# Kernel optimization log

Hardware: AMD Instinct MI355X
Metric: run time of the kernel (lower is better)

Reference implementation:

```python
import jax, jax.numpy as jnp
import numpy as np
import math

HEAD_SIZE = 128
N_EMBED = 2048
B, T = 4, 4096
TOP_K_RATIO = 0.1


def setup_inputs() -> dict:
    key = jax.random.key(0)
    k1, k2, k3, k4 = jax.random.split(key, 4)
    index = jax.random.normal(k1, (B, T, N_EMBED), dtype=jnp.float32)
    s = 1.0 / math.sqrt(N_EMBED)
    Wq = jax.random.normal(k2, (N_EMBED, HEAD_SIZE), dtype=jnp.float32) * s
    Wk = jax.random.normal(k3, (N_EMBED, HEAD_SIZE), dtype=jnp.float32) * s
    Wv = jax.random.normal(k4, (N_EMBED, HEAD_SIZE), dtype=jnp.float32) * s
    return {"index": index, "Wq": Wq, "Wk": Wk, "Wv": Wv}


def reference(index, Wq, Wk, Wv):
    # memory = index (self-attention case)
    Bv, Tv, _ = index.shape
    top_k = int(TOP_K_RATIO * Tv)  # 409

    q = index @ Wq  # [B, T, D]
    k = index @ Wk
    v = index @ Wv

    q_norms = jnp.linalg.norm(q, axis=-1)  # [B, T]
    _, top_idx = jax.lax.top_k(q_norms, top_k)  # [B, K]

    idx = top_idx[..., None]  # [B, K, 1]
    q_topk = jnp.take_along_axis(q, idx, axis=1)  # [B, K, D]
    k_topk = jnp.take_along_axis(k, idx, axis=1)
    v_topk = jnp.take_along_axis(v, idx, axis=1)

    w = jnp.einsum('bid,bjd->bij', q_topk, k_topk) / math.sqrt(HEAD_SIZE)
    # eval mode: no causal mask (only applied in training), dropout = identity
    w = jax.nn.softmax(w, axis=-1)  # stable softmax (internal max subtraction)
    out_topk = w @ v_topk  # [B, K, D]

    batch_idx = jnp.arange(Bv)[:, None]  # [B, 1]
    output = jnp.zeros((Bv, Tv, HEAD_SIZE), dtype=out_topk.dtype)
    output = output.at[batch_idx, top_idx].add(out_topk)  # scatter_add (indices unique)
    return output
```

## Files before the change

### kernel.cpp

```cpp
#include <hip/hip_runtime.h>
#include <hip/hip_bf16.h>

#define NB 4
#define NT 4096
#define NC 2048
#define ND 128
#define NK 409
#define KPAD 416

#define BM 32
#define BK 32
#define ASTR 40
#define BSTR 40

typedef __attribute__((ext_vector_type(8))) short short8;
typedef __attribute__((ext_vector_type(4))) float f32x4;

__device__ __forceinline__ void split2(float x, ushort& h, ushort& l) {
    union { float f; unsigned u; } a; a.f = x;
    unsigned r = a.u + 0x7FFFu + ((a.u >> 16) & 1u);
    h = (ushort)(r >> 16);
    union { unsigned u; float f; } hb; hb.u = ((unsigned)h) << 16;
    float res = x - hb.f;
    union { float f; unsigned u; } b; b.f = res;
    unsigned r2 = b.u + 0x7FFFu + ((b.u >> 16) & 1u);
    l = (ushort)(r2 >> 16);
}

__device__ __forceinline__ uint2 pack4(const ushort* s) {
    uint2 v;
    v.x = (unsigned)s[0] | ((unsigned)s[1] << 16);
    v.y = (unsigned)s[2] | ((unsigned)s[3] << 16);
    return v;
}

__device__ __forceinline__ uint4 pack8(const ushort* s) {
    uint4 v;
    v.x = (unsigned)s[0] | ((unsigned)s[1] << 16);
    v.y = (unsigned)s[2] | ((unsigned)s[3] << 16);
    v.z = (unsigned)s[4] | ((unsigned)s[5] << 16);
    v.w = (unsigned)s[6] | ((unsigned)s[7] << 16);
    return v;
}

__global__ __launch_bounds__(256) void bconv_kernel(
    const float* __restrict__ Wq, ushort* __restrict__ Bhi, ushort* __restrict__ Blo)
{
    const int t = threadIdx.x;
    const int n = t & 127;
    const int kk0 = blockIdx.x * 32 + (t >> 7) * 16;
    ushort hb[16], lb[16];
    #pragma unroll
    for (int j = 0; j < 16; ++j) {
        float x = Wq[(size_t)(kk0 + j) * ND + n];
        split2(x, hb[j], lb[j]);
    }
    *(uint4*)&Bhi[(size_t)n * NC + kk0 + 0] = pack8(hb);
    *(uint4*)&Bhi[(size_t)n * NC + kk0 + 8] = pack8(hb + 8);
    *(uint4*)&Blo[(size_t)n * NC + kk0 + 0] = pack8(lb);
    *(uint4*)&Blo[(size_t)n * NC + kk0 + 8] = pack8(lb + 8);
}

__global__ __launch_bounds__(256) void bconv_kv_kernel(
    const float* __restrict__ Wk, const float* __restrict__ Wv,
    ushort* __restrict__ Bhi, ushort* __restrict__ Blo)
{
    const float* __restrict__ W = blockIdx.y ? Wv : Wk;
    const int t = threadIdx.x;
    const int n = t & 127;
    const int nr = blockIdx.y * 128 + n;
    const int kk0 = blockIdx.x * 32 + (t >> 7) * 16;
    ushort hb[16], lb[16];
    #pragma unroll
    for (int j = 0; j < 16; ++j) {
        float x = W[(size_t)(kk0 + j) * ND + n];
        split2(x, hb[j], lb[j]);
    }
    *(uint4*)&Bhi[(size_t)nr * NC + kk0 + 0] = pack8(hb);
    *(uint4*)&Bhi[(size_t)nr * NC + kk0 + 8] = pack8(hb + 8);
    *(uint4*)&Blo[(size_t)nr * NC + kk0 + 0] = pack8(lb);
    *(uint4*)&Blo[(size_t)nr * NC + kk0 + 8] = pack8(lb + 8);
}

__global__ __launch_bounds__(256, 2) void qgemm_mfma(
    const float* __restrict__ A, const ushort* __restrict__ Bhi,
    const ushort* __restrict__ Blo, float* __restrict__ q)
{
    __shared__ ushort Ah[BM * ASTR];
    __shared__ ushort Al[BM * ASTR];
    __shared__ ushort Bh[128 * BSTR];
    __shared__ ushort Bl[128 * BSTR];

    const int tid  = threadIdx.x;
    const int m0   = blockIdx.x * BM;
    const int w    = tid >> 6;
    const int lane = tid & 63;
    const int wm   = w >> 1, wn = w & 1;
    const int lrow = lane & 15, lq = lane >> 4;

    const int ar = tid >> 3, ak = (tid & 7) * 4;
    const float* aptr = A + (size_t)(m0 + ar) * NC + ak;
    const int br = tid >> 1, bk = (tid & 1) * 16;
    const ushort* bhp = Bhi + (size_t)br * NC + bk;
    const ushort* blp = Blo + (size_t)br * NC + bk;

    f32x4 acc[4];
    #pragma unroll
    for (int j = 0; j < 4; ++j) acc[j] = (f32x4){0.f, 0.f, 0.f, 0.f};

    for (int k0 = 0; k0 < NC; k0 += BK) {
        float4 f0 = *(const float4*)(aptr + k0);
        uint4 bh0 = *(const uint4*)(bhp + k0);
        uint4 bh1 = *(const uint4*)(bhp + k0 + 8);
        uint4 bl0 = *(const uint4*)(blp + k0);
        uint4 bl1 = *(const uint4*)(blp + k0 + 8);
        ushort h[4], l[4];
        split2(f0.x, h[0], l[0]);
        split2(f0.y, h[1], l[1]);
        split2(f0.z, h[2], l[2]);
        split2(f0.w, h[3], l[3]);

        __syncthreads();
        *(uint2*)&Ah[ar * ASTR + ak] = pack4(h);
        *(uint2*)&Al[ar * ASTR + ak] = pack4(l);
        *(uint4*)&Bh[br * BSTR + bk + 0] = bh0;
        *(uint4*)&Bh[br * BSTR + bk + 8] = bh1;
        *(uint4*)&Bl[br * BSTR + bk + 0] = bl0;
        *(uint4*)&Bl[br * BSTR + bk + 8] = bl1;
        __syncthreads();

        const int row = wm * 16 + lrow;
        short8 ah = *(const short8*)&Ah[row * ASTR + lq * 8];
        short8 al = *(const short8*)&Al[row * ASTR + lq * 8];
        #pragma unroll
        for (int ni = 0; ni < 4; ++ni) {
            const int n = wn * 64 + ni * 16 + lrow;
            short8 bhf = *(const short8*)&Bh[n * BSTR + lq * 8];
            short8 blf = *(const short8*)&Bl[n * BSTR + lq * 8];
            acc[ni] = __builtin_amdgcn_mfma_f32_16x16x32_bf16(ah, bhf, acc[ni], 0, 0, 0);
            acc[ni] = __builtin_amdgcn_mfma_f32_16x16x32_bf16(ah, blf, acc[ni], 0, 0, 0);
            acc[ni] = __builtin_amdgcn_mfma_f32_16x16x32_bf16(al, bhf, acc[ni], 0, 0, 0);
        }
    }

    #pragma unroll
    for (int ni = 0; ni < 4; ++ni) {
        const int col = wn * 64 + ni * 16 + lrow;
        #pragma unroll
        for (int r = 0; r < 4; ++r) {
            const int grow = m0 + wm * 16 + lq * 4 + r;
            q[(size_t)grow * ND + col] = acc[ni][r];
        }
    }
}

__global__ __launch_bounds__(256, 2) void kvgemm_mfma(
    const float* __restrict__ X, const ushort* __restrict__ Bhi,
    const ushort* __restrict__ Blo, const int* __restrict__ topi,
    float* __restrict__ ktop, float* __restrict__ vtop)
{
    __shared__ ushort Ah[BM * ASTR];
    __shared__ ushort Al[BM * ASTR];
    __shared__ ushort Bh[128 * BSTR];
    __shared__ ushort Bl[128 * BSTR];

    const int tid  = threadIdx.x;
    const int m0   = blockIdx.x * BM;
    const int w    = tid >> 6;
    const int lane = tid & 63;
    const int wm   = w >> 1, wn = w & 1;
    const int lrow = lane & 15, lq = lane >> 4;

    const int ar = tid >> 3, ak = (tid & 7) * 4;
    int gi = m0 + ar;
    int giC = gi < NB * NK ? gi : NB * NK - 1;
    int b = giC / NK, ii = giC % NK;
    int srow = topi[b * KPAD + ii];
    const float* aptr = X + ((size_t)b * NT + srow) * NC + ak;

    const int br = tid >> 1, bk = (tid & 1) * 16;
    const ushort* bhp = Bhi + (size_t)(blockIdx.y * 128 + br) * NC + bk;
    const ushort* blp = Blo + (size_t)(blockIdx.y * 128 + br) * NC + bk;

    f32x4 acc[4];
    #pragma unroll
    for (int j = 0; j < 4; ++j) acc[j] = (f32x4){0.f, 0.f, 0.f, 0.f};

    for (int k0 = 0; k0 < NC; k0 += BK) {
        float4 f0 = *(const float4*)(aptr + k0);
        uint4 bh0 = *(const uint4*)(bhp + k0);
        uint4 bh1 = *(const uint4*)(bhp + k0 + 8);
        uint4 bl0 = *(const uint4*)(blp + k0);
        uint4 bl1 = *(const uint4*)(blp + k0 + 8);
        ushort h[4], l[4];
        split2(f0.x, h[0], l[0]);
        split2(f0.y, h[1], l[1]);
        split2(f0.z, h[2], l[2]);
        split2(f0.w, h[3], l[3]);

        __syncthreads();
        *(uint2*)&Ah[ar * ASTR + ak] = pack4(h);
        *(uint2*)&Al[ar * ASTR + ak] = pack4(l);
        *(uint4*)&Bh[br * BSTR + bk + 0] = bh0;
        *(uint4*)&Bh[br * BSTR + bk + 8] = bh1;
        *(uint4*)&Bl[br * BSTR + bk + 0] = bl0;
        *(uint4*)&Bl[br * BSTR + bk + 8] = bl1;
        __syncthreads();

        const int row = wm * 16 + lrow;
        short8 ah = *(const short8*)&Ah[row * ASTR + lq * 8];
        short8 al = *(const short8*)&Al[row * ASTR + lq * 8];
        #pragma unroll
        for (int ni = 0; ni < 4; ++ni) {
            const int n = wn * 64 + ni * 16 + lrow;
            short8 bhf = *(const short8*)&Bh[n * BSTR + lq * 8];
            short8 blf = *(const short8*)&Bl[n * BSTR + lq * 8];
            acc[ni] = __builtin_amdgcn_mfma_f32_16x16x32_bf16(ah, bhf, acc[ni], 0, 0, 0);
            acc[ni] = __builtin_amdgcn_mfma_f32_16x16x32_bf16(ah, blf, acc[ni], 0, 0, 0);
            acc[ni] = __builtin_amdgcn_mfma_f32_16x16x32_bf16(al, bhf, acc[ni], 0, 0, 0);
        }
    }

    float* __restrict__ dst = blockIdx.y ? vtop : ktop;
    #pragma unroll
    for (int ni = 0; ni < 4; ++ni) {
        const int col = wn * 64 + ni * 16 + lrow;
        #pragma unroll
        for (int r = 0; r < 4; ++r) {
            const int grow = m0 + wm * 16 + lq * 4 + r;
            if (grow < NB * NK)
                dst[(size_t)grow * ND + col] = acc[ni][r];
        }
    }
}

__global__ __launch_bounds__(256) void qnorm_kernel(
    const float* __restrict__ q, float* __restrict__ qn)
{
    const int wv = (blockIdx.x * 256 + threadIdx.x) >> 6;
    const int lane = threadIdx.x & 63;
    const float* r = q + (size_t)wv * ND;
    float a = r[lane], b = r[lane + 64];
    float s = a * a + b * b;
    #pragma unroll
    for (int off = 32; off > 0; off >>= 1) s += __shfl_xor(s, off);
    if (lane == 0) qn[wv] = sqrtf(s);
}

__global__ __launch_bounds__(256) void topk_kernel(
    const float* __restrict__ qn, int* __restrict__ topi, int* __restrict__ cnt)
{
    __shared__ int rs[4][64];
    const int b = blockIdx.y;
    const int is = threadIdx.x & 63;
    const int i = blockIdx.x * 64 + is;
    const int chunk = threadIdx.x >> 6;
    const float vi = qn[(size_t)b * NT + i];
    const float4* qv = (const float4*)(qn + (size_t)b * NT + chunk * 1024);
    int rank = 0;
    #pragma unroll 4
    for (int j4 = 0; j4 < 256; ++j4) {
        float4 v = qv[j4];
        int j = chunk * 1024 + j4 * 4;
        rank += (v.x > vi || (v.x == vi && (j + 0) < i)) ? 1 : 0;
        rank += (v.y > vi || (v.y == vi && (j + 1) < i)) ? 1 : 0;
        rank += (v.z > vi || (v.z == vi && (j + 2) < i)) ? 1 : 0;
        rank += (v.w > vi || (v.w == vi && (j + 3) < i)) ? 1 : 0;
    }
    rs[chunk][is] = rank;
    __syncthreads();
    if (threadIdx.x < 64) {
        int rk = rs[0][threadIdx.x] + rs[1][threadIdx.x] + rs[2][threadIdx.x] + rs[3][threadIdx.x];
        if (rk < NK) {
            int p = atomicAdd(&cnt[b], 1);
            topi[b * KPAD + p] = blockIdx.x * 64 + threadIdx.x;
        }
    }
}

__global__ __launch_bounds__(256) void attn_kernel(
    const float* __restrict__ q, const float* __restrict__ ktop,
    const float* __restrict__ vtop, const int* __restrict__ topi,
    float* __restrict__ out)
{
    __shared__ float qs[ND];
    __shared__ float ss[KPAD];
    __shared__ float red[256];
    __shared__ float pv[2][ND];
    const int bi = blockIdx.x;
    const int b = bi / NK, i = bi % NK;
    const int t = threadIdx.x;
    const int row = topi[b * KPAD + i];
    if (t < ND) qs[t] = q[((size_t)b * NT + row) * ND + t];
    __syncthreads();

    const float scale = 0.08838834764831844f;
    float mymax = -1e30f;
    #pragma unroll
    for (int rep = 0; rep < 2; ++rep) {
        int j = t + rep * 256;
        if (j < NK) {
            const float4* kr = (const float4*)(ktop + ((size_t)b * NK + j) * ND);
            const float4* q4 = (const float4*)qs;
            float s = 0.f;
            #pragma unroll
            for (int dd = 0; dd < 32; ++dd) {
                float4 a = q4[dd], kv = kr[dd];
                s += a.x * kv.x + a.y * kv.y + a.z * kv.z + a.w * kv.w;
            }
            s *= scale;
            ss[j] = s;
            mymax = fmaxf(mymax, s);
        }
    }
    red[t] = mymax;
    __syncthreads();
    for (int off = 128; off > 0; off >>= 1) {
        if (t < off) red[t] = fmaxf(red[t], red[t + off]);
        __syncthreads();
    }
    const float mx = red[0];
    __syncthreads();

    float mysum = 0.f;
    #pragma unroll
    for (int rep = 0; rep < 2; ++rep) {
        int j = t + rep * 256;
        if (j < NK) {
            float p = __expf(ss[j] - mx);
            ss[j] = p;
            mysum += p;
        }
    }
    red[t] = mysum;
    __syncthreads();
    for (int off = 128; off > 0; off >>= 1) {
        if (t < off) red[t] += red[t + off];
        __syncthreads();
    }
    const float inv = 1.f / red[0];

    const int col = t & (ND - 1), half = t >> 7;
    float o = 0.f;
    #pragma unroll 4
    for (int j = half; j < NK; j += 2)
        o = fmaf(ss[j], vtop[((size_t)b * NK + j) * ND + col], o);
    pv[half][col] = o;
    __syncthreads();
    if (t < ND)
        out[((size_t)b * NT + row) * ND + t] = (pv[0][t] + pv[1][t]) * inv;
}

extern "C" void kernel_launch(void* const* d_in, const int* in_sizes, int n_in,
                              void* d_out, int out_size, void* d_ws, size_t ws_size,
                              hipStream_t stream)
{
    const float* index = (const float*)d_in[0];
    const float* Wq = (const float*)d_in[1];
    const float* Wk = (const float*)d_in[2];
    const float* Wv = (const float*)d_in[3];
    float* out = (float*)d_out;

    char* ws = (char*)d_ws;
    float*  q    = (float*)(ws);
    float*  qn   = (float*)(ws + 8388608);
    int*    topi = (int*)  (ws + 8454144);
    int*    cnt  = (int*)  (ws + 8462336);
    float*  ktop = (float*)(ws + 8462592);
    float*  vtop = (float*)(ws + 9300224);

    ushort* Bqhi  = (ushort*)d_out;
    ushort* Bqlo  = (ushort*)((char*)d_out + 524288);
    ushort* Bkvhi = (ushort*)d_out;
    ushort* Bkvlo = (ushort*)((char*)d_out + 1048576);

    hipMemsetAsync(cnt, 0, NB * sizeof(int), stream);

    bconv_kernel<<<dim3(NC / 32), dim3(256), 0, stream>>>(Wq, Bqhi, Bqlo);
    qgemm_mfma<<<dim3(NB * NT / BM), dim3(256), 0, stream>>>(index, Bqhi, Bqlo, q);
    qnorm_kernel<<<dim3(NB * NT / 4), dim3(256), 0, stream>>>(q, qn);
    topk_kernel<<<dim3(NT / 64, NB), dim3(256), 0, stream>>>(qn, topi, cnt);
    bconv_kv_kernel<<<dim3(NC / 32, 2), dim3(256), 0, stream>>>(Wk, Wv, Bkvhi, Bkvlo);
    kvgemm_mfma<<<dim3((NB * NK + BM - 1) / BM, 2), dim3(256), 0, stream>>>(
        index, Bkvhi, Bkvlo, topi, ktop, vtop);
    hipMemsetAsync(d_out, 0, (size_t)out_size * sizeof(float), stream);
    attn_kernel<<<dim3(NB * NK), dim3(256), 0, stream>>>(q, ktop, vtop, topi, out);
}
```

Baseline: 413.5 us.

## Split-K the Q GEMM, prefetch global tiles, and shrink KV GEMM tiles

The Q projection GEMM is split along K into two halves over a second grid dimension. The partial results go to two buffers and are summed inside the norm kernel, which also writes the combined q back. Both GEMMs now prefetch the next K tile into registers before the MFMA work, a register double-buffer that overlaps global loads with compute. The KV GEMM uses 16-row tiles so more blocks fill the GPU for the small gathered problem. This adds an extra read and write of q and moves the Wq bf16 buffers into the workspace, which overlaps ktop, already consumed by then.

```diff
diff --git a/kernel.cpp b/kernel.cpp
--- a/kernel.cpp
+++ b/kernel.cpp
@@ -27,19 +27,23 @@
     l = (ushort)(r2 >> 16);
 }
 
+__device__ __forceinline__ unsigned pack2(ushort a, ushort b) {
+    return (unsigned)a | ((unsigned)b << 16);
+}
+
 __device__ __forceinline__ uint2 pack4(const ushort* s) {
     uint2 v;
-    v.x = (unsigned)s[0] | ((unsigned)s[1] << 16);
-    v.y = (unsigned)s[2] | ((unsigned)s[3] << 16);
+    v.x = pack2(s[0], s[1]);
+    v.y = pack2(s[2], s[3]);
     return v;
 }
 
 __device__ __forceinline__ uint4 pack8(const ushort* s) {
     uint4 v;
-    v.x = (unsigned)s[0] | ((unsigned)s[1] << 16);
-    v.y = (unsigned)s[2] | ((unsigned)s[3] << 16);
-    v.z = (unsigned)s[4] | ((unsigned)s[5] << 16);
-    v.w = (unsigned)s[6] | ((unsigned)s[7] << 16);
+    v.x = pack2(s[0], s[1]);
+    v.y = pack2(s[2], s[3]);
+    v.z = pack2(s[4], s[5]);
+    v.w = pack2(s[6], s[7]);
     return v;
 }
 
@@ -82,9 +86,10 @@
     *(uint4*)&Blo[(size_t)nr * NC + kk0 + 8] = pack8(lb + 8);
 }
 
-__global__ __launch_bounds__(256, 2) void qgemm_mfma(
+__global__ __launch_bounds__(256, 4) void qgemm_mfma(
     const float* __restrict__ A, const ushort* __restrict__ Bhi,
-    const ushort* __restrict__ Blo, float* __restrict__ q)
+    const ushort* __restrict__ Blo, float* __restrict__ q1,
+    float* __restrict__ q2)
 {
     __shared__ ushort Ah[BM * ASTR];
     __shared__ ushort Al[BM * ASTR];
@@ -93,41 +98,53 @@
 
     const int tid  = threadIdx.x;
     const int m0   = blockIdx.x * BM;
+    const int kb   = blockIdx.y * (NC / 2);
     const int w    = tid >> 6;
     const int lane = tid & 63;
     const int wm   = w >> 1, wn = w & 1;
     const int lrow = lane & 15, lq = lane >> 4;
 
     const int ar = tid >> 3, ak = (tid & 7) * 4;
-    const float* aptr = A + (size_t)(m0 + ar) * NC + ak;
+    const float* aptr = A + (size_t)(m0 + ar) * NC + kb + ak;
     const int br = tid >> 1, bk = (tid & 1) * 16;
-    const ushort* bhp = Bhi + (size_t)br * NC + bk;
-    const ushort* blp = Blo + (size_t)br * NC + bk;
+    const ushort* bhp = Bhi + (size_t)br * NC + kb + bk;
+    const ushort* blp = Blo + (size_t)br * NC + kb + bk;
 
     f32x4 acc[4];
     #pragma unroll
     for (int j = 0; j < 4; ++j) acc[j] = (f32x4){0.f, 0.f, 0.f, 0.f};
 
-    for (int k0 = 0; k0 < NC; k0 += BK) {
-        float4 f0 = *(const float4*)(aptr + k0);
-        uint4 bh0 = *(const uint4*)(bhp + k0);
-        uint4 bh1 = *(const uint4*)(bhp + k0 + 8);
-        uint4 bl0 = *(const uint4*)(blp + k0);
-        uint4 bl1 = *(const uint4*)(blp + k0 + 8);
+    const int KITER = (NC / 2) / BK;
+    float4 fA = *(const float4*)(aptr);
+    uint4 vb0 = *(const uint4*)(bhp);
+    uint4 vb1 = *(const uint4*)(bhp + 8);
+    uint4 vb2 = *(const uint4*)(blp);
+    uint4 vb3 = *(const uint4*)(blp + 8);
+
+    for (int kt = 0; kt < KITER; ++kt) {
         ushort h[4], l[4];
-        split2(f0.x, h[0], l[0]);
-        split2(f0.y, h[1], l[1]);
-        split2(f0.z, h[2], l[2]);
-        split2(f0.w, h[3], l[3]);
+        split2(fA.x, h[0], l[0]);
+        split2(fA.y, h[1], l[1]);
+        split2(fA.z, h[2], l[2]);
+        split2(fA.w, h[3], l[3]);
 
         __syncthreads();
         *(uint2*)&Ah[ar * ASTR + ak] = pack4(h);
         *(uint2*)&Al[ar * ASTR + ak] = pack4(l);
-        *(uint4*)&Bh[br * BSTR + bk + 0] = bh0;
-        *(uint4*)&Bh[br * BSTR + bk + 8] = bh1;
-        *(uint4*)&Bl[br * BSTR + bk + 0] = bl0;
-        *(uint4*)&Bl[br * BSTR + bk + 8] = bl1;
-        __syncthreads();
+        *(uint4*)&Bh[br * BSTR + bk + 0] = vb0;
+        *(uint4*)&Bh[br * BSTR + bk + 8] = vb1;
+        *(uint4*)&Bl[br * BSTR + bk + 0] = vb2;
+        *(uint4*)&Bl[br * BSTR + bk + 8] = vb3;
+        __syncthreads();
+
+        if (kt + 1 < KITER) {
+            const int off = (kt + 1) * BK;
+            fA  = *(const float4*)(aptr + off);
+            vb0 = *(const uint4*)(bhp + off);
+            vb1 = *(const uint4*)(bhp + off + 8);
+            vb2 = *(const uint4*)(blp + off);
+            vb3 = *(const uint4*)(blp + off + 8);
+        }
 
         const int row = wm * 16 + lrow;
         short8 ah = *(const short8*)&Ah[row * ASTR + lq * 8];
@@ -143,13 +160,14 @@
         }
     }
 
+    float* __restrict__ qdst = blockIdx.y ? q2 : q1;
     #pragma unroll
     for (int ni = 0; ni < 4; ++ni) {
         const int col = wn * 64 + ni * 16 + lrow;
         #pragma unroll
         for (int r = 0; r < 4; ++r) {
             const int grow = m0 + wm * 16 + lq * 4 + r;
-            q[(size_t)grow * ND + col] = acc[ni][r];
+            qdst[(size_t)grow * ND + col] = acc[ni][r];
         }
     }
 }
@@ -159,19 +177,18 @@
     const ushort* __restrict__ Blo, const int* __restrict__ topi,
     float* __restrict__ ktop, float* __restrict__ vtop)
 {
-    __shared__ ushort Ah[BM * ASTR];
-    __shared__ ushort Al[BM * ASTR];
+    __shared__ ushort Ah[16 * ASTR];
+    __shared__ ushort Al[16 * ASTR];
     __shared__ ushort Bh[128 * BSTR];
     __shared__ ushort Bl[128 * BSTR];
 
     const int tid  = threadIdx.x;
-    const int m0   = blockIdx.x * BM;
+    const int m0   = blockIdx.x * 16;
     const int w    = tid >> 6;
     const int lane = tid & 63;
-    const int wm   = w >> 1, wn = w & 1;
     const int lrow = lane & 15, lq = lane >> 4;
 
-    const int ar = tid >> 3, ak = (tid & 7) * 4;
+    const int ar = tid >> 4, ak = (tid & 15) * 2;
     int gi = m0 + ar;
     int giC = gi < NB * NK ? gi : NB * NK - 1;
     int b = giC / NK, ii = giC % NK;
@@ -182,37 +199,45 @@
     const ushort* bhp = Bhi + (size_t)(blockIdx.y * 128 + br) * NC + bk;
     const ushort* blp = Blo + (size_t)(blockIdx.y * 128 + br) * NC + bk;
 
-    f32x4 acc[4];
-    #pragma unroll
-    for (int j = 0; j < 4; ++j) acc[j] = (f32x4){0.f, 0.f, 0.f, 0.f};
-
-    for (int k0 = 0; k0 < NC; k0 += BK) {
-        float4 f0 = *(const float4*)(aptr + k0);
-        uint4 bh0 = *(const uint4*)(bhp + k0);
-        uint4 bh1 = *(const uint4*)(bhp + k0 + 8);
-        uint4 bl0 = *(const uint4*)(blp + k0);
-        uint4 bl1 = *(const uint4*)(blp + k0 + 8);
-        ushort h[4], l[4];
-        split2(f0.x, h[0], l[0]);
-        split2(f0.y, h[1], l[1]);
-        split2(f0.z, h[2], l[2]);
-        split2(f0.w, h[3], l[3]);
-
-        __syncthreads();
-        *(uint2*)&Ah[ar * ASTR + ak] = pack4(h);
-        *(uint2*)&Al[ar * ASTR + ak] = pack4(l);
-        *(uint4*)&Bh[br * BSTR + bk + 0] = bh0;
-        *(uint4*)&Bh[br * BSTR + bk + 8] = bh1;
-        *(uint4*)&Bl[br * BSTR + bk + 0] = bl0;
-        *(uint4*)&Bl[br * BSTR + bk + 8] = bl1;
-        __syncthreads();
-
-        const int row = wm * 16 + lrow;
-        short8 ah = *(const short8*)&Ah[row * ASTR + lq * 8];
-        short8 al = *(const short8*)&Al[row * ASTR + lq * 8];
+    f32x4 acc[2];
+    acc[0] = (f32x4){0.f, 0.f, 0.f, 0.f};
+    acc[1] = (f32x4){0.f, 0.f, 0.f, 0.f};
+
+    const int KITER = NC / BK;
+    float2 fA = *(const float2*)(aptr);
+    uint4 vb0 = *(const uint4*)(bhp);
+    uint4 vb1 = *(const uint4*)(bhp + 8);
+    uint4 vb2 = *(const uint4*)(blp);
+    uint4 vb3 = *(const uint4*)(blp + 8);
+
+    for (int kt = 0; kt < KITER; ++kt) {
+        ushort h[2], l[2];
+        split2(fA.x, h[0], l[0]);
+        split2(fA.y, h[1], l[1]);
+
+        __syncthreads();
+        *(unsigned*)&Ah[ar * ASTR + ak] = pack2(h[0], h[1]);
+        *(unsigned*)&Al[ar * ASTR + ak] = pack2(l[0], l[1]);
+        *(uint4*)&Bh[br * BSTR + bk + 0] = vb0;
+        *(uint4*)&Bh[br * BSTR + bk + 8] = vb1;
+        *(uint4*)&Bl[br * BSTR + bk + 0] = vb2;
+        *(uint4*)&Bl[br * BSTR + bk + 8] = vb3;
+        __syncthreads();
+
+        if (kt + 1 < KITER) {
+            const int off = (kt + 1) * BK;
+            fA  = *(const float2*)(aptr + off);
+            vb0 = *(const uint4*)(bhp + off);
+            vb1 = *(const uint4*)(bhp + off + 8);
+            vb2 = *(const uint4*)(blp + off);
+            vb3 = *(const uint4*)(blp + off + 8);
+        }
+
+        short8 ah = *(const short8*)&Ah[lrow * ASTR + lq * 8];
+        short8 al = *(const short8*)&Al[lrow * ASTR + lq * 8];
         #pragma unroll
-        for (int ni = 0; ni < 4; ++ni) {
-            const int n = wn * 64 + ni * 16 + lrow;
+        for (int ni = 0; ni < 2; ++ni) {
+            const int n = w * 32 + ni * 16 + lrow;
             short8 bhf = *(const short8*)&Bh[n * BSTR + lq * 8];
             short8 blf = *(const short8*)&Bl[n * BSTR + lq * 8];
             acc[ni] = __builtin_amdgcn_mfma_f32_16x16x32_bf16(ah, bhf, acc[ni], 0, 0, 0);
@@ -223,11 +248,11 @@
 
     float* __restrict__ dst = blockIdx.y ? vtop : ktop;
     #pragma unroll
-    for (int ni = 0; ni < 4; ++ni) {
-        const int col = wn * 64 + ni * 16 + lrow;
+    for (int ni = 0; ni < 2; ++ni) {
+        const int col = w * 32 + ni * 16 + lrow;
         #pragma unroll
         for (int r = 0; r < 4; ++r) {
-            const int grow = m0 + wm * 16 + lq * 4 + r;
+            const int grow = m0 + lq * 4 + r;
             if (grow < NB * NK)
                 dst[(size_t)grow * ND + col] = acc[ni][r];
         }
@@ -235,12 +260,16 @@
 }
 
 __global__ __launch_bounds__(256) void qnorm_kernel(
-    const float* __restrict__ q, float* __restrict__ qn)
+    float* __restrict__ q1, const float* __restrict__ q2, float* __restrict__ qn)
 {
     const int wv = (blockIdx.x * 256 + threadIdx.x) >> 6;
     const int lane = threadIdx.x & 63;
-    const float* r = q + (size_t)wv * ND;
-    float a = r[lane], b = r[lane + 64];
+    float* r1 = q1 + (size_t)wv * ND;
+    const float* r2 = q2 + (size_t)wv * ND;
+    float a = r1[lane] + r2[lane];
+    float b = r1[lane + 64] + r2[lane + 64];
+    r1[lane] = a;
+    r1[lane + 64] = b;
     float s = a * a + b * b;
     #pragma unroll
     for (int off = 32; off > 0; off >>= 1) s += __shfl_xor(s, off);
@@ -362,27 +391,28 @@
     float* out = (float*)d_out;
 
     char* ws = (char*)d_ws;
-    float*  q    = (float*)(ws);
+    float*  q1   = (float*)(ws);
     float*  qn   = (float*)(ws + 8388608);
     int*    topi = (int*)  (ws + 8454144);
     int*    cnt  = (int*)  (ws + 8462336);
+    ushort* Bqhi = (ushort*)(ws + 8462592);
+    ushort* Bqlo = (ushort*)(ws + 8986880);
     float*  ktop = (float*)(ws + 8462592);
     float*  vtop = (float*)(ws + 9300224);
 
-    ushort* Bqhi  = (ushort*)d_out;
-    ushort* Bqlo  = (ushort*)((char*)d_out + 524288);
+    float*  q2    = (float*)d_out;
     ushort* Bkvhi = (ushort*)d_out;
     ushort* Bkvlo = (ushort*)((char*)d_out + 1048576);
 
     hipMemsetAsync(cnt, 0, NB * sizeof(int), stream);
 
     bconv_kernel<<<dim3(NC / 32), dim3(256), 0, stream>>>(Wq, Bqhi, Bqlo);
-    qgemm_mfma<<<dim3(NB * NT / BM), dim3(256), 0, stream>>>(index, Bqhi, Bqlo, q);
-    qnorm_kernel<<<dim3(NB * NT / 4), dim3(256), 0, stream>>>(q, qn);
+    qgemm_mfma<<<dim3(NB * NT / BM, 2), dim3(256), 0, stream>>>(index, Bqhi, Bqlo, q1, q2);
+    qnorm_kernel<<<dim3(NB * NT / 4), dim3(256), 0, stream>>>(q1, q2, qn);
     topk_kernel<<<dim3(NT / 64, NB), dim3(256), 0, stream>>>(qn, topi, cnt);
     bconv_kv_kernel<<<dim3(NC / 32, 2), dim3(256), 0, stream>>>(Wk, Wv, Bkvhi, Bkvlo);
-    kvgemm_mfma<<<dim3((NB * NK + BM - 1) / BM, 2), dim3(256), 0, stream>>>(
+    kvgemm_mfma<<<dim3((NB * NK + 15) / 16, 2), dim3(256), 0, stream>>>(
         index, Bkvhi, Bkvlo, topi, ktop, vtop);
     hipMemsetAsync(d_out, 0, (size_t)out_size * sizeof(float), stream);
-    attn_kernel<<<dim3(NB * NK), dim3(256), 0, stream>>>(q, ktop, vtop, topi, out);
-}
+    attn_kernel<<<dim3(NB * NK), dim3(256), 0, stream>>>(q1, ktop, vtop, topi, out);
+}
```

Result: no change. 406.3 us (-1.7%).
